# Performance work log

Hardware: AMD Instinct MI355X
Metric: run time of the kernel (lower is better)

Reference implementation:

```python
import jax, jax.numpy as jnp
import numpy as np

DN = ('NCHW', 'OIHW', 'NCHW')

def conv2d(x, w, b):
    y = jax.lax.conv_general_dilated(x, w, window_strides=(1, 1), padding='SAME', dimension_numbers=DN)
    return y + b[None, :, None, None]

def setup_inputs() -> dict:
    key = jax.random.key(0)
    ks = jax.random.split(key, 8)
    C = 256
    Cq = C // 8
    B, H, W = 8, 56, 56
    fan_out_qk = Cq * 9
    fan_out_v = C * 9
    std_qk = np.sqrt(2.0 / fan_out_qk)  # kaiming_normal fan_out, relu
    std_v = np.sqrt(2.0 / fan_out_v)
    return {
        'x': jax.random.normal(ks[0], (B, C, H, W), dtype=jnp.float32),
        'wq': jax.random.normal(ks[1], (Cq, C, 3, 3), dtype=jnp.float32) * std_qk,
        'bq': jnp.zeros((Cq,), dtype=jnp.float32),
        'wk': jax.random.normal(ks[2], (Cq, C, 3, 3), dtype=jnp.float32) * std_qk,
        'bk': jnp.zeros((Cq,), dtype=jnp.float32),
        'wv': jax.random.normal(ks[3], (C, C, 3, 3), dtype=jnp.float32) * std_v,
        'bv': jnp.zeros((C,), dtype=jnp.float32),
        'gamma': jax.random.uniform(ks[4], (1,), dtype=jnp.float32) * 0.1,
    }

def reference(x, wq, bq, wk, bk, wv, bv, gamma):
    B, C, H, W = x.shape
    N = H * W
    q = conv2d(x, wq, bq).reshape(B, -1, N)   # [B, C/8, N]
    k = conv2d(x, wk, bk).reshape(B, -1, N)   # [B, C/8, N]
    v = conv2d(x, wv, bv).reshape(B, C, N)    # [B, C, N]
    # energy[b,i,j] = sum_d q[b,d,i] * k[b,d,j]  (unscaled)
    energy = jnp.einsum('bdi,bdj->bij', q, k)
    attention = jax.nn.softmax(energy, axis=-1)  # [B, N, N]
    # out[b,c,i] = sum_j v[b,c,j] * attention[b,i,j]
    out = jnp.einsum('bcj,bij->bci', v, attention).reshape(B, C, H, W)
    return gamma[0] * out + x
```

## Files before the change

### kernel.cpp

```cpp
#include <hip/hip_runtime.h>
#include <math.h>

#define B_ 8
#define C_ 256
#define H_ 56
#define W_ 56
#define N_ 3136
#define BN_ (B_*N_)
#define LOG2E 1.44269504088896340736f

typedef __attribute__((ext_vector_type(8))) short short8;
typedef __attribute__((ext_vector_type(4))) float f32x4;
typedef __attribute__((ext_vector_type(16))) float f32x16;
typedef __attribute__((ext_vector_type(4))) unsigned short u16x4;
#define MFMA16(A, Bf, Cf) __builtin_amdgcn_mfma_f32_16x16x32_bf16((A), (Bf), (Cf), 0, 0, 0)
#define MFMA32(A, Bf, Cf) __builtin_amdgcn_mfma_f32_32x32x16_bf16((A), (Bf), (Cf), 0, 0, 0)

#define XT_ELEMS (B_*58*64*256)
#define A_ELEMS  (320*2304)
#define AHI_OFF  (2*XT_ELEMS)
#define ALO_OFF  (AHI_OFF + A_ELEMS)
#define QKT_HI_OFF (ALO_OFF + A_ELEMS)
#define QKT_ELEMS  (B_*N_*64)
#define QKT_LO_OFF (QKT_HI_OFF + QKT_ELEMS)
#define VBF_OFF    (QKT_LO_OFF + QKT_ELEMS)
#define VBF_ELEMS  (B_*C_*N_)

#define QF_ELEMS (B_*196*64*8)


#define SX(col) ((((col) & 3)) ^ (((col) >> 2) & 3))
#define SWZ(r, col, c8) ((((r)*64 + (col))*4) + ((c8) ^ SX(col)))

#define PSTR 76
#define VSTR 58

__device__ inline unsigned short f2bf(float f) {
    unsigned u = __float_as_uint(f);
    unsigned r = (u + 0x7fffu + ((u >> 16) & 1u)) >> 16;
    return (unsigned short)r;
}
__device__ inline float bf2f(unsigned short h) {
    return __uint_as_float(((unsigned)h) << 16);
}
__device__ inline float exp2_hw(float x) {
    float r; asm("v_exp_f32 %0, %1" : "=v"(r) : "v"(x)); return r;
}
__device__ inline unsigned cvt_pk_bf16(float lo, float hi) {
    unsigned r; asm("v_cvt_pk_bf16_f32 %0, %1, %2" : "=v"(r) : "v"(lo), "v"(hi)); return r;
}
__device__ inline void gl_lds16(const unsigned short* g, uint4* l) {
    __builtin_amdgcn_global_load_lds(
        (const __attribute__((address_space(1))) unsigned int*)g,
        (__attribute__((address_space(3))) unsigned int*)l,
        16, 0, 0);
}

__global__ __launch_bounds__(256) void zero_pads(
    unsigned short* __restrict__ xhi, unsigned short* __restrict__ xlo)
{
    const int g = blockIdx.x*256 + threadIdx.x;
    const int half = 61440;
    unsigned short* base = (g < half) ? xhi : xlo;
    const int i = (g < half) ? g : g - half;
    const int b = i / 7680, rem = i - b*7680;
    const int slot = rem >> 5, c8 = rem & 31;
    int row, col;
    if (slot < 64)       { row = 0;  col = slot; }
    else if (slot < 128) { row = 57; col = slot - 64; }
    else if (slot < 184) { row = slot - 127; col = 0; }
    else                 { row = slot - 183; col = 57; }
    const size_t o = ((size_t)((b*58 + row)*64 + col))*256 + c8*8;
    *(uint4*)(base + o) = make_uint4(0, 0, 0, 0);
}

__global__ __launch_bounds__(256) void prep_x(
    const float* __restrict__ x,
    unsigned short* __restrict__ xhi, unsigned short* __restrict__ xlo)
{
    __shared__ float xs[64][57];
    const int cc = blockIdx.x, y = blockIdx.y, b = blockIdx.z;
    const int t = threadIdx.x;
    const int c0 = cc * 64;
    for (int idx = t; idx < 64 * 56; idx += 256) {
        const int ch = idx / 56, xc = idx - ch * 56;
        xs[ch][xc] = x[((size_t)(b*C_ + c0 + ch)*H_ + y)*W_ + xc];
    }
    __syncthreads();
    for (int idx = t; idx < 56 * 32; idx += 256) {
        const int xc = idx >> 5, chp = idx & 31;
        const float v0 = xs[2*chp][xc], v1 = xs[2*chp + 1][xc];
        const unsigned short h0 = f2bf(v0), h1 = f2bf(v1);
        const unsigned short l0 = f2bf(v0 - bf2f(h0));
        const unsigned short l1 = f2bf(v1 - bf2f(h1));
        const size_t o = ((size_t)(b*58 + y + 1) * 64 + (xc + 1)) * 256 + c0 + 2*chp;
        *(unsigned*)(xhi + o) = (unsigned)h0 | ((unsigned)h1 << 16);
        *(unsigned*)(xlo + o) = (unsigned)l0 | ((unsigned)l1 << 16);
    }
}

__global__ __launch_bounds__(256) void prep_w(
    const float* __restrict__ wq, const float* __restrict__ wk,
    const float* __restrict__ wv,
    unsigned short* __restrict__ Ahi, unsigned short* __restrict__ Alo)
{
    const int g = blockIdx.x * 256 + threadIdx.x;
    if (g >= 320 * 2304) return;
    const int m = g / 2304, k = g - m * 2304;
    const int s = k >> 8, c = k & 255;
    float w;
    if (m < 32)      w = wq[((size_t)m*C_ + c)*9 + s];
    else if (m < 64) w = wk[((size_t)(m-32)*C_ + c)*9 + s];
    else             w = wv[((size_t)(m-64)*C_ + c)*9 + s];
    const unsigned short h = f2bf(w);
    const int cc = (k >> 5) & 7, quad = (k >> 3) & 3, e = k & 7;
    const size_t o = ((((size_t)(m >> 4)*9 + s)*8 + cc)*64 + (quad*16 + (m & 15)))*8 + e;
    Ahi[o] = h;
    Alo[o] = f2bf(w - bf2f(h));
}

__global__ __launch_bounds__(256, 3) void conv_fused(
    const unsigned short* __restrict__ xhi, const unsigned short* __restrict__ xlo,
    const unsigned short* __restrict__ Ahi, const unsigned short* __restrict__ Alo,
    const float* __restrict__ bq, const float* __restrict__ bk,
    const float* __restrict__ bv,
    unsigned short* __restrict__ qkt_hi, unsigned short* __restrict__ qkt_lo,
    unsigned short* __restrict__ vbf)
{
    __shared__ uint4 SMEM[3080];
    const int b = blockIdx.x, y = blockIdx.y, z = blockIdx.z;
    const int t = threadIdx.x;
    const int w = t >> 6, L = t & 63;
    const int ln = L & 15, quad = L >> 4;

    size_t gofs[3];
#pragma unroll
    for (int i = 0; i < 3; i++) {
        const int ci = w*192 + i*64 + L;
        const int r = ci >> 8, col = (ci >> 2) & 63;
        const int c8 = (ci & 3) ^ SX(col);
        gofs[i] = ((size_t)((b*58 + y + r)*64 + col))*256 + c8*8;
    }

    if (z == 0) {
        const int wrg = w >> 1, wnt = w & 1;
        f32x4 acc[2][2];
#pragma unroll
        for (int i = 0; i < 2; i++) { acc[i][0] = (f32x4)0.0f; acc[i][1] = (f32x4)0.0f; }

#pragma unroll
        for (int i = 0; i < 3; i++) {
            gl_lds16(xhi + gofs[i], SMEM + w*192 + i*64);
            gl_lds16(xlo + gofs[i], SMEM + 768 + w*192 + i*64);
        }
        __syncthreads();

        for (int cc = 0; cc < 8; cc++) {
            const int buf = cc & 1;
            const uint4* sH = SMEM + buf*1536;
            const uint4* sL = sH + 768;
            if (cc < 7) {
                uint4* nB = SMEM + (buf^1)*1536;
#pragma unroll
                for (int i = 0; i < 3; i++) {
                    gl_lds16(xhi + gofs[i] + (cc+1)*32, nB + w*192 + i*64);
                    gl_lds16(xlo + gofs[i] + (cc+1)*32, nB + 768 + w*192 + i*64);
                }
            }
#pragma unroll
            for (int s = 0; s < 9; s++) {
                const int dx = s % 3 - 1;
                const int r = s / 3;
                short8 ah[2], al[2];
#pragma unroll
                for (int rgi = 0; rgi < 2; rgi++) {
                    const int rg = wrg*2 + rgi;
                    const size_t aoff = (((size_t)(rg*9 + s)*8 + cc)*64 + L)*8;
                    ah[rgi] = *(const short8*)(Ahi + aoff);
                    al[rgi] = *(const short8*)(Alo + aoff);
                }
#pragma unroll
                for (int nti = 0; nti < 2; nti++) {
                    const int col = (wnt*2 + nti)*16 + ln + dx + 1;
                    const int i4 = SWZ(r, col, quad);
                    const short8 bh = *(const short8*)&sH[i4];
                    const short8 bl = *(const short8*)&sL[i4];
#pragma unroll
                    for (int rgi = 0; rgi < 2; rgi++) {
                        acc[rgi][nti] = MFMA16(ah[rgi], bh, acc[rgi][nti]);
                        acc[rgi][nti] = MFMA16(ah[rgi], bl, acc[rgi][nti]);
                        acc[rgi][nti] = MFMA16(al[rgi], bh, acc[rgi][nti]);
                    }
                }
            }
            if (cc < 7) __syncthreads();
        }

#pragma unroll
        for (int rgi = 0; rgi < 2; rgi++) {
            const int rg = wrg*2 + rgi;
            const int m0 = rg*16 + quad*4;
#pragma unroll
            for (int nti = 0; nti < 2; nti++) {
                const int px = (wnt*2 + nti)*16 + ln;
                if (px >= 56) continue;
                const int pix = y*56 + px;
                u16x4 hi4, lo4;
#pragma unroll
                for (int r = 0; r < 4; r++) {
                    const int m = m0 + r;
                    const float bias = (m < 32) ? bq[m] : bk[m - 32];
                    float val = acc[rgi][nti][r] + bias;
                    if (rg < 2) val *= LOG2E;
                    const unsigned short h = f2bf(val);
                    hi4[r] = h;
                    lo4[r] = f2bf(val - bf2f(h));
                }
                size_t o;
                if (rg < 2) {
                    o = ((size_t)(b*196 + (pix >> 4))*64 + (m0 >> 3)*16 + (pix & 15))*8 + (m0 & 7);
                } else {
                    const int mk0 = m0 - 32;
                    o = (size_t)QF_ELEMS +
                        (((size_t)(b*49 + (pix >> 6))*4 + ((pix >> 4) & 3))*64
                         + (mk0 >> 3)*16 + (pix & 15))*8 + (mk0 & 7);
                }
                *(u16x4*)(qkt_hi + o) = hi4;
                *(u16x4*)(qkt_lo + o) = lo4;
            }
        }
    } else {
        f32x4 acc[4][4];
#pragma unroll
        for (int rg = 0; rg < 4; rg++)
#pragma unroll
            for (int nt = 0; nt < 4; nt++) acc[rg][nt] = (f32x4)0.0f;

#pragma unroll
        for (int i = 0; i < 3; i++)
            gl_lds16(xhi + gofs[i], SMEM + w*192 + i*64);
        __syncthreads();

        for (int cc = 0; cc < 8; cc++) {
            const int buf = cc & 1;
            const uint4* sH = SMEM + buf*768;
            if (cc < 7) {
                uint4* nB = SMEM + (buf^1)*768;
#pragma unroll
                for (int i = 0; i < 3; i++)
                    gl_lds16(xhi + gofs[i] + (cc+1)*32, nB + w*192 + i*64);
            }
#pragma unroll
            for (int s = 0; s < 9; s++) {
                const int dx = s % 3 - 1;
                const int r = s / 3;
                short8 a[4];
#pragma unroll
                for (int rg = 0; rg < 4; rg++) {
                    const size_t aoff = (((size_t)((4 + w*4 + rg)*9 + s)*8 + cc)*64 + L)*8;
                    a[rg] = *(const short8*)(Ahi + aoff);
                }
#pragma unroll
                for (int nt = 0; nt < 4; nt++) {
                    const int col = nt*16 + ln + dx + 1;
                    const short8 bf = *(const short8*)&sH[SWZ(r, col, quad)];
#pragma unroll
                    for (int rg = 0; rg < 4; rg++)
                        acc[rg][nt] = MFMA16(a[rg], bf, acc[rg][nt]);
                }
            }
            __syncthreads();
        }

        unsigned short* Vs = (unsigned short*)SMEM;
#pragma unroll
        for (int rg = 0; rg < 4; rg++)
#pragma unroll
            for (int nt = 0; nt < 4; nt++) {
                const int px = nt*16 + ln;
                if (px >= 56) continue;
#pragma unroll
                for (int r = 0; r < 4; r++) {
                    const int cl = (w*4 + rg)*16 + quad*4 + r;
                    Vs[cl*VSTR + px] = f2bf(acc[rg][nt][r] + bv[cl]);
                }
            }
        __syncthreads();
        const int p0 = y*56;
        const int hh = L >> 5, c31 = L & 31;
        const int gend = (p0 + 55) >> 4;
        for (int gi = p0 >> 4; gi <= gend; gi++) {
            const int pxl0 = gi*16 + hh*8 - p0;
            if (pxl0 >= 0 && pxl0 + 8 <= 56) {
#pragma unroll
                for (int cgk = 0; cgk < 2; cgk++) {
                    const int cg = w*2 + cgk;
                    const short8 vv = *(const short8*)&Vs[(cg*32 + c31)*VSTR + pxl0];
                    const size_t o = ((((size_t)(b*8 + cg)*49 + (gi >> 2))*4 + (gi & 3))*64 + L)*8;
                    *(short8*)(vbf + o) = vv;
                }
            }
        }
    }
}

__global__ __launch_bounds__(128, 4) void attn_flash2w(
    const unsigned short* __restrict__ qkt_hi, const unsigned short* __restrict__ qkt_lo,
    const unsigned short* __restrict__ vbf,
    const float* __restrict__ x, const float* __restrict__ gptr,
    float* __restrict__ out)
{
    __shared__ unsigned short P[2][32*PSTR];
    __shared__ float alphaL[2][32];
    __shared__ float lL[32];

    const int bx = blockIdx.x;
    const int b = bx & 7, it = bx >> 3;
    const int chalf = blockIdx.y;
    const int i_base = it * 32;
    const int t = threadIdx.x;
    const int w = t >> 6, L = t & 63;
    const int ln = L & 15, quad = L >> 4;
    const int l32 = L & 31, h32 = L >> 5;

    const unsigned short* Kf_hi = qkt_hi + QF_ELEMS;
    const unsigned short* Kf_lo = qkt_lo + QF_ELEMS;

    const size_t qoff = ((size_t)(b*196 + it*2 + w)*64 + L)*8;
    const short8 qh = *(const short8*)(qkt_hi + qoff);
    const short8 ql = *(const short8*)(qkt_lo + qoff);

    float m_run = -INFINITY, l_run = 0.0f;
    f32x16 O0 = (f32x16)0.0f, O1 = (f32x16)0.0f;
    const int cg0 = chalf*4 + w*2;
    const unsigned short* vt0 = vbf + ((size_t)(b*8 + cg0)*49)*2048 + (size_t)L*8;
    const unsigned short* vt1 = vt0 + (size_t)49*2048;
    const unsigned short* kbh = Kf_hi + (size_t)b*49*2048 + (size_t)L*8;
    const unsigned short* kbl = Kf_lo + (size_t)b*49*2048 + (size_t)L*8;

    for (int jt = 0; jt < 49; jt++) {
        const int buf = jt & 1;

        short8 Va[4], Vb[4];
#pragma unroll
        for (int s = 0; s < 4; s++) {
            Va[s] = *(const short8*)(vt0 + jt*2048 + s*512);
            Vb[s] = *(const short8*)(vt1 + jt*2048 + s*512);
        }

        f32x4 sacc[4];
#pragma unroll
        for (int tj = 0; tj < 4; tj++) {
            const short8 kh = *(const short8*)(kbh + jt*2048 + tj*512);
            const short8 kl = *(const short8*)(kbl + jt*2048 + tj*512);
            f32x4 a = (f32x4)0.0f;
            a = MFMA16(kh, qh, a);
            a = MFMA16(kh, ql, a);
            a = MFMA16(kl, qh, a);
            sacc[tj] = a;
        }
        float mt0 = fmaxf(fmaxf(sacc[0][0], sacc[0][1]), fmaxf(sacc[0][2], sacc[0][3]));
        float mt1 = fmaxf(fmaxf(sacc[1][0], sacc[1][1]), fmaxf(sacc[1][2], sacc[1][3]));
        float mt2 = fmaxf(fmaxf(sacc[2][0], sacc[2][1]), fmaxf(sacc[2][2], sacc[2][3]));
        float mt3 = fmaxf(fmaxf(sacc[3][0], sacc[3][1]), fmaxf(sacc[3][2], sacc[3][3]));
        float mx = fmaxf(fmaxf(mt0, mt1), fmaxf(mt2, mt3));
        mx = fmaxf(mx, __shfl_xor(mx, 16));
        mx = fmaxf(mx, __shfl_xor(mx, 32));

        float alpha = 1.0f;
        if (__any(mx > m_run + 8.0f)) {
            const float m_new = fmaxf(m_run, mx);
            alpha = exp2_hw(m_run - m_new);
            m_run = m_new;
        }

#pragma unroll
        for (int tj = 0; tj < 4; tj++)
#pragma unroll
            for (int r = 0; r < 4; r++)
                sacc[tj][r] = exp2_hw(sacc[tj][r] - m_run);
        float s0 = (sacc[0][0] + sacc[0][1]) + (sacc[0][2] + sacc[0][3]);
        float s1 = (sacc[1][0] + sacc[1][1]) + (sacc[1][2] + sacc[1][3]);
        float s2 = (sacc[2][0] + sacc[2][1]) + (sacc[2][2] + sacc[2][3]);
        float s3 = (sacc[3][0] + sacc[3][1]) + (sacc[3][2] + sacc[3][3]);
        float ps = (s0 + s1) + (s2 + s3);
        ps += __shfl_xor(ps, 16);
        ps += __shfl_xor(ps, 32);
        l_run = l_run * alpha + ps;

        {
            unsigned short* prow = &P[buf][(w*16 + ln)*PSTR];
#pragma unroll
            for (int tj = 0; tj < 4; tj++) {
                uint2 pp;
                pp.x = cvt_pk_bf16(sacc[tj][0], sacc[tj][1]);
                pp.y = cvt_pk_bf16(sacc[tj][2], sacc[tj][3]);
                *(uint2*)(prow + tj*16 + quad*4) = pp;
            }
        }
        if (quad == 0) alphaL[buf][w*16 + ln] = alpha;

        __syncthreads();

        const float a = alphaL[buf][l32];
        if (__any(a != 1.0f)) {
#pragma unroll
            for (int rg = 0; rg < 16; rg++) { O0[rg] *= a; O1[rg] *= a; }
        }
        short8 Bp[4];
#pragma unroll
        for (int s = 0; s < 4; s++) {
            Bp[s] = *(const short8*)&P[buf][l32*PSTR + s*16 + h32*8];
            O0 = MFMA32(Va[s], Bp[s], O0);
        }
#pragma unroll
        for (int s = 0; s < 4; s++)
            O1 = MFMA32(Vb[s], Bp[s], O1);
    }

    __syncthreads();
    if (quad == 0) lL[w*16 + ln] = l_run;
    __syncthreads();
    const float inv = gptr[0] / lL[l32];

    const int pix = i_base + l32;
#pragma unroll
    for (int g = 0; g < 2; g++) {
        const f32x16 Ot = g ? O1 : O0;
        const int cg = chalf*128 + w*64 + g*32;
#pragma unroll
        for (int reg = 0; reg < 16; reg++) {
            const int c = cg + (reg & 3) + 8*(reg >> 2) + 4*h32;
            const size_t idx = (size_t)(b*C_ + c)*N_ + pix;
            out[idx] = x[idx] + inv * Ot[reg];
        }
    }
}

extern "C" void kernel_launch(void* const* d_in, const int* in_sizes, int n_in,
                              void* d_out, int out_size, void* d_ws, size_t ws_size,
                              hipStream_t stream)
{
    (void)in_sizes; (void)n_in; (void)out_size; (void)ws_size;
    const float* x  = (const float*)d_in[0];
    const float* wq = (const float*)d_in[1];
    const float* bq = (const float*)d_in[2];
    const float* wk = (const float*)d_in[3];
    const float* bk = (const float*)d_in[4];
    const float* wv = (const float*)d_in[5];
    const float* bv = (const float*)d_in[6];
    const float* gm = (const float*)d_in[7];
    float* out = (float*)d_out;

    unsigned short* u = (unsigned short*)d_ws;
    unsigned short* xhi = u;
    unsigned short* xlo = u + XT_ELEMS;
    unsigned short* Ahi = u + AHI_OFF;
    unsigned short* Alo = u + ALO_OFF;
    unsigned short* qkt_hi = u + QKT_HI_OFF;
    unsigned short* qkt_lo = u + QKT_LO_OFF;
    unsigned short* vbf = u + VBF_OFF;

    hipLaunchKernelGGL(zero_pads, dim3(480), dim3(256), 0, stream, xhi, xlo);
    hipLaunchKernelGGL(prep_x, dim3(4, 56, 8), dim3(256), 0, stream, x, xhi, xlo);
    hipLaunchKernelGGL(prep_w, dim3(2880), dim3(256), 0, stream, wq, wk, wv, Ahi, Alo);
    hipLaunchKernelGGL(conv_fused, dim3(8, 56, 2), dim3(256), 0, stream,
                       xhi, xlo, Ahi, Alo, bq, bk, bv, qkt_hi, qkt_lo, vbf);
    hipLaunchKernelGGL(attn_flash2w, dim3(98*8, 2), dim3(128), 0, stream,
                       qkt_hi, qkt_lo, vbf, x, gm, out);
}
```

Before: 295.5 us.

## Prefetch K tiles in attention, merge prep kernels, use lighter LDS barrier

Merges zero_pads and prep_w into one prep_misc launch, removing a kernel launch. In the attention loop, the next iteration's K hi/lo fragments are loaded into registers after the QK MFMAs, so global load latency overlaps the softmax and PV work. The __syncthreads is replaced by an explicit lgkmcnt wait plus s_barrier, which does not wait on the outstanding global loads. Launch bounds are relaxed from 4 to 3 waves to make room for the extra registers, which may lower occupancy.

```diff
diff --git a/kernel.cpp b/kernel.cpp
--- a/kernel.cpp
+++ b/kernel.cpp
@@ -55,23 +55,47 @@
         (__attribute__((address_space(3))) unsigned int*)l,
         16, 0, 0);
 }
-
-__global__ __launch_bounds__(256) void zero_pads(
-    unsigned short* __restrict__ xhi, unsigned short* __restrict__ xlo)
+__device__ inline void lds_barrier() {
+    asm volatile("s_waitcnt lgkmcnt(0)" ::: "memory");
+    __builtin_amdgcn_s_barrier();
+    asm volatile("" ::: "memory");
+}
+
+__global__ __launch_bounds__(256) void prep_misc(
+    unsigned short* __restrict__ xhi, unsigned short* __restrict__ xlo,
+    const float* __restrict__ wq, const float* __restrict__ wk,
+    const float* __restrict__ wv,
+    unsigned short* __restrict__ Ahi, unsigned short* __restrict__ Alo)
 {
-    const int g = blockIdx.x*256 + threadIdx.x;
-    const int half = 61440;
-    unsigned short* base = (g < half) ? xhi : xlo;
-    const int i = (g < half) ? g : g - half;
-    const int b = i / 7680, rem = i - b*7680;
-    const int slot = rem >> 5, c8 = rem & 31;
-    int row, col;
-    if (slot < 64)       { row = 0;  col = slot; }
-    else if (slot < 128) { row = 57; col = slot - 64; }
-    else if (slot < 184) { row = slot - 127; col = 0; }
-    else                 { row = slot - 183; col = 57; }
-    const size_t o = ((size_t)((b*58 + row)*64 + col))*256 + c8*8;
-    *(uint4*)(base + o) = make_uint4(0, 0, 0, 0);
+    if (blockIdx.x < 480) {
+        const int g = blockIdx.x*256 + threadIdx.x;
+        const int half = 61440;
+        unsigned short* base = (g < half) ? xhi : xlo;
+        const int i = (g < half) ? g : g - half;
+        const int b = i / 7680, rem = i - b*7680;
+        const int slot = rem >> 5, c8 = rem & 31;
+        int row, col;
+        if (slot < 64)       { row = 0;  col = slot; }
+        else if (slot < 128) { row = 57; col = slot - 64; }
+        else if (slot < 184) { row = slot - 127; col = 0; }
+        else                 { row = slot - 183; col = 57; }
+        const size_t o = ((size_t)((b*58 + row)*64 + col))*256 + c8*8;
+        *(uint4*)(base + o) = make_uint4(0, 0, 0, 0);
+    } else {
+        const int g = (blockIdx.x - 480)*256 + threadIdx.x;
+        if (g >= 320 * 2304) return;
+        const int m = g / 2304, k = g - m * 2304;
+        const int s = k >> 8, c = k & 255;
+        float w;
+        if (m < 32)      w = wq[((size_t)m*C_ + c)*9 + s];
+        else if (m < 64) w = wk[((size_t)(m-32)*C_ + c)*9 + s];
+        else             w = wv[((size_t)(m-64)*C_ + c)*9 + s];
+        const unsigned short h = f2bf(w);
+        const int cc = (k >> 5) & 7, quad = (k >> 3) & 3, e = k & 7;
+        const size_t o = ((((size_t)(m >> 4)*9 + s)*8 + cc)*64 + (quad*16 + (m & 15)))*8 + e;
+        Ahi[o] = h;
+        Alo[o] = f2bf(w - bf2f(h));
+    }
 }
 
 __global__ __launch_bounds__(256) void prep_x(
@@ -97,26 +121,6 @@
         *(unsigned*)(xhi + o) = (unsigned)h0 | ((unsigned)h1 << 16);
         *(unsigned*)(xlo + o) = (unsigned)l0 | ((unsigned)l1 << 16);
     }
-}
-
-__global__ __launch_bounds__(256) void prep_w(
-    const float* __restrict__ wq, const float* __restrict__ wk,
-    const float* __restrict__ wv,
-    unsigned short* __restrict__ Ahi, unsigned short* __restrict__ Alo)
-{
-    const int g = blockIdx.x * 256 + threadIdx.x;
-    if (g >= 320 * 2304) return;
-    const int m = g / 2304, k = g - m * 2304;
-    const int s = k >> 8, c = k & 255;
-    float w;
-    if (m < 32)      w = wq[((size_t)m*C_ + c)*9 + s];
-    else if (m < 64) w = wk[((size_t)(m-32)*C_ + c)*9 + s];
-    else             w = wv[((size_t)(m-64)*C_ + c)*9 + s];
-    const unsigned short h = f2bf(w);
-    const int cc = (k >> 5) & 7, quad = (k >> 3) & 3, e = k & 7;
-    const size_t o = ((((size_t)(m >> 4)*9 + s)*8 + cc)*64 + (quad*16 + (m & 15)))*8 + e;
-    Ahi[o] = h;
-    Alo[o] = f2bf(w - bf2f(h));
 }
 
 __global__ __launch_bounds__(256, 3) void conv_fused(
@@ -304,7 +308,7 @@
     }
 }
 
-__global__ __launch_bounds__(128, 4) void attn_flash2w(
+__global__ __launch_bounds__(128, 3) void attn_flash2w(
     const unsigned short* __restrict__ qkt_hi, const unsigned short* __restrict__ qkt_lo,
     const unsigned short* __restrict__ vbf,
     const float* __restrict__ x, const float* __restrict__ gptr,
@@ -338,6 +342,13 @@
     const unsigned short* kbh = Kf_hi + (size_t)b*49*2048 + (size_t)L*8;
     const unsigned short* kbl = Kf_lo + (size_t)b*49*2048 + (size_t)L*8;
 
+    short8 kh[4], kl[4];
+#pragma unroll
+    for (int tj = 0; tj < 4; tj++) {
+        kh[tj] = *(const short8*)(kbh + tj*512);
+        kl[tj] = *(const short8*)(kbl + tj*512);
+    }
+
     for (int jt = 0; jt < 49; jt++) {
         const int buf = jt & 1;
 
@@ -351,14 +362,21 @@
         f32x4 sacc[4];
 #pragma unroll
         for (int tj = 0; tj < 4; tj++) {
-            const short8 kh = *(const short8*)(kbh + jt*2048 + tj*512);
-            const short8 kl = *(const short8*)(kbl + jt*2048 + tj*512);
             f32x4 a = (f32x4)0.0f;
-            a = MFMA16(kh, qh, a);
-            a = MFMA16(kh, ql, a);
-            a = MFMA16(kl, qh, a);
+            a = MFMA16(kh[tj], qh, a);
+            a = MFMA16(kh[tj], ql, a);
+            a = MFMA16(kl[tj], qh, a);
             sacc[tj] = a;
         }
+
+        if (jt < 48) {
+#pragma unroll
+            for (int tj = 0; tj < 4; tj++) {
+                kh[tj] = *(const short8*)(kbh + (jt+1)*2048 + tj*512);
+                kl[tj] = *(const short8*)(kbl + (jt+1)*2048 + tj*512);
+            }
+        }
+
         float mt0 = fmaxf(fmaxf(sacc[0][0], sacc[0][1]), fmaxf(sacc[0][2], sacc[0][3]));
         float mt1 = fmaxf(fmaxf(sacc[1][0], sacc[1][1]), fmaxf(sacc[1][2], sacc[1][3]));
         float mt2 = fmaxf(fmaxf(sacc[2][0], sacc[2][1]), fmaxf(sacc[2][2], sacc[2][3]));
@@ -400,7 +418,7 @@
         }
         if (quad == 0) alphaL[buf][w*16 + ln] = alpha;
 
-        __syncthreads();
+        lds_barrier();
 
         const float a = alphaL[buf][l32];
         if (__any(a != 1.0f)) {
@@ -461,9 +479,9 @@
     unsigned short* qkt_lo = u + QKT_LO_OFF;
     unsigned short* vbf = u + VBF_OFF;
 
-    hipLaunchKernelGGL(zero_pads, dim3(480), dim3(256), 0, stream, xhi, xlo);
+    hipLaunchKernelGGL(prep_misc, dim3(3360), dim3(256), 0, stream,
+                       xhi, xlo, wq, wk, wv, Ahi, Alo);
     hipLaunchKernelGGL(prep_x, dim3(4, 56, 8), dim3(256), 0, stream, x, xhi, xlo);
-    hipLaunchKernelGGL(prep_w, dim3(2880), dim3(256), 0, stream, wq, wk, wv, Ahi, Alo);
     hipLaunchKernelGGL(conv_fused, dim3(8, 56, 2), dim3(256), 0, stream,
                        xhi, xlo, Ahi, Alo, bq, bk, bv, qkt_hi, qkt_lo, vbf);
     hipLaunchKernelGGL(attn_flash2w, dim3(98*8, 2), dim3(128), 0, stream,
```

Result: slower. 307.8 us (+4.2%).
